# Kernel tuning notes

Measured on AMD Instinct MI355X. Metric: run time of the kernel, lower is better.

## Reference

```python
import jax, jax.numpy as jnp
import numpy as np

B = 8192
D_IN = 2048
MM = 1600
CHUNKS = 20
CS = MM // CHUNKS  # 80
D_OUT = 3000
EPS = 1e-12  # F.normalize clamp eps


def setup_inputs() -> dict:
    key = jax.random.key(0)
    ks = jax.random.split(key, 10)
    s_in = 1.0 / np.sqrt(D_IN)
    s_c = 1.0 / np.sqrt(CS)
    s_mm = 1.0 / np.sqrt(MM)
    return {
        "x0": jax.random.normal(ks[0], (B, D_IN), jnp.float32),
        "x1": jax.random.normal(ks[1], (B, D_IN), jnp.float32),
        "W0": jax.random.uniform(ks[2], (D_IN, MM), jnp.float32, -s_in, s_in),
        "b0": jax.random.uniform(ks[3], (MM,), jnp.float32, -s_in, s_in),
        "W1": jax.random.uniform(ks[4], (D_IN, MM), jnp.float32, -s_in, s_in),
        "b1": jax.random.uniform(ks[5], (MM,), jnp.float32, -s_in, s_in),
        # stacked bilinear weights: [chunks, out, in1, in2] like torch Bilinear
        "Wb": jax.random.uniform(ks[6], (CHUNKS, CS, CS, CS), jnp.float32, -s_c, s_c),
        "bb": jax.random.uniform(ks[7], (CHUNKS, CS), jnp.float32, -s_c, s_c),
        "Wout": jax.random.uniform(ks[8], (MM, D_OUT), jnp.float32, -s_mm, s_mm),
        "bout": jax.random.uniform(ks[9], (D_OUT,), jnp.float32, -s_mm, s_mm),
    }


def reference(x0, x1, W0, b0, W1, b1, Wb, bb, Wout, bout):
    # input projections: [B, MM]
    h0 = x0 @ W0 + b0
    h1 = x1 @ W1 + b1
    # split into equal chunks: [B, CHUNKS, CS]
    h0c = h0.reshape(B, CHUNKS, CS)
    h1c = h1.reshape(B, CHUNKS, CS)
    # batched bilinear over all chunks: z[b,c,o] = sum_{s,t} h0[b,c,s] Wb[c,o,s,t] h1[b,c,t] + bb[c,o]
    z = jnp.einsum('bcs,cost,bct->bco', h0c, Wb, h1c) + bb[None, :, :]
    # signed sqrt (pos_norm == 'before_cat')
    z = jnp.sqrt(jax.nn.relu(z)) - jnp.sqrt(jax.nn.relu(-z))
    # L2 normalize per chunk (torch F.normalize over dim=1 of the [B, CS] chunk)
    norm = jnp.linalg.norm(z, axis=-1, keepdims=True)
    z = z / jnp.maximum(norm, EPS)
    # concat chunks -> [B, MM], final projection
    z = z.reshape(B, MM)
    return z @ Wout + bout
```

## Files before the change

kernel.cpp:

```cpp
#include <hip/hip_runtime.h>
#include <hip/hip_bf16.h>

typedef unsigned short u16;
typedef unsigned int   u32;

using bf16x8 = __attribute__((ext_vector_type(8))) short;
using f32x4  = __attribute__((ext_vector_type(4))) float;
using fvec4  = __attribute__((ext_vector_type(4))) float;
using u16x4  = __attribute__((ext_vector_type(4))) unsigned short;

#define BSZ   8192
#define DIN   2048
#define MMD   1600
#define NCH   20
#define CSZ   80
#define DOUT  3000

__device__ __forceinline__ float bf2f(u16 u) {
    u32 x = ((u32)u) << 16; float f; __builtin_memcpy(&f, &x, 4); return f;
}
__device__ __forceinline__ u16 f2bf(float f) {
    u32 x; __builtin_memcpy(&x, &f, 4);
    u32 r = x + 0x7fffu + ((x >> 16) & 1u);
    return (u16)(r >> 16);
}

__device__ __forceinline__ void gl2lds16(const void* g, const void* l) {
    __builtin_amdgcn_global_load_lds(
        (const __attribute__((address_space(1))) u32*)g,
        (__attribute__((address_space(3))) u32*)l, 16, 0, 0);
}

__global__ void cast_bf16_k(const float* __restrict__ src, u16* __restrict__ dst, int n4) {
    int i = blockIdx.x * blockDim.x + threadIdx.x;
    if (i < n4) {
        fvec4 v = ((const fvec4*)src)[i];
        u16x4 o;
        o.x = f2bf(v.x); o.y = f2bf(v.y); o.z = f2bf(v.z); o.w = f2bf(v.w);
        ((u16x4*)dst)[i] = o;
    }
}

__global__ void transpose_cast_k(const float* __restrict__ src, u16* __restrict__ dst,
                                 int K, int N) {
    __shared__ float t[32][33];
    int k0 = blockIdx.x * 32, n0 = blockIdx.y * 32;
    int tx = threadIdx.x & 31, ty = threadIdx.x >> 5;
#pragma unroll
    for (int r = 0; r < 4; r++) {
        int n = n0 + tx;
        float v = (n < N) ? src[(size_t)(k0 + ty + 8 * r) * N + n] : 0.f;
        t[ty + 8 * r][tx] = v;
    }
    __syncthreads();
#pragma unroll
    for (int r = 0; r < 4; r++)
        dst[(size_t)(n0 + ty + 8 * r) * K + k0 + tx] = f2bf(t[tx][ty + 8 * r]);
}

template<bool OUT_BF16>
__global__ __launch_bounds__(256, 2) void gemm_bt_k(
    const u16* __restrict__ A, const u16* __restrict__ BT,
    const float* __restrict__ bias, void* __restrict__ C, int K, int N) {
    __shared__ __align__(16) u16 As[128 * 64];
    __shared__ __align__(16) u16 Bs[128 * 64];
    const int tid = threadIdx.x, w = tid >> 6, lane = tid & 63;
    const int lr = lane & 15, lk = lane >> 4, s7 = lr & 7;
    const int m0 = blockIdx.x * 128, n0 = blockIdx.y * 128;
    const int mh = (w >> 1) * 64, nh = (w & 1) * 64;
    const int so = (lane & 7) ^ (lane >> 3);
    int arow[4], brow[4];
#pragma unroll
    for (int i = 0; i < 4; i++) { arow[i] = (mh + i * 16 + lr) * 64; brow[i] = (nh + i * 16 + lr) * 64; }
    f32x4 acc[4][4] = {};
    const u16* Ag = A + (size_t)m0 * K;
    const u16* Bg = BT + (size_t)n0 * K;
    const int nslab = K >> 6;
    for (int kt = 0; kt < nslab; ++kt) {
        const int k0 = kt * 64;
        __syncthreads();
#pragma unroll
        for (int q = 0; q < 4; q++) {
            int ch = w * 4 + q;
            int row = ch * 8 + (lane >> 3);
            gl2lds16(Ag + (size_t)row * K + k0 + so * 8, As + ch * 512);
            gl2lds16(Bg + (size_t)row * K + k0 + so * 8, Bs + ch * 512);
        }
        __syncthreads();
#pragma unroll
        for (int ks = 0; ks < 64; ks += 32) {
            const int px = (((ks >> 3) + lk) ^ s7) * 8;
            bf16x8 av[4], bv[4];
#pragma unroll
            for (int i = 0; i < 4; i++) av[i] = *(const bf16x8*)(As + arow[i] + px);
#pragma unroll
            for (int j = 0; j < 4; j++) bv[j] = *(const bf16x8*)(Bs + brow[j] + px);
#pragma unroll
            for (int i = 0; i < 4; i++)
#pragma unroll
                for (int j = 0; j < 4; j++)
                    acc[i][j] = __builtin_amdgcn_mfma_f32_16x16x32_bf16(av[i], bv[j], acc[i][j], 0, 0, 0);
        }
    }
#pragma unroll
    for (int j = 0; j < 4; j++) {
        int n = n0 + nh + j * 16 + lr;
        if (n < N) {
            float bv = bias[n];
#pragma unroll
            for (int i = 0; i < 4; i++) {
                int mb = m0 + mh + i * 16 + lk * 4;
#pragma unroll
                for (int r = 0; r < 4; r++) {
                    float v = acc[i][j][r] + bv;
                    if (OUT_BF16) ((u16*)C)[(size_t)(mb + r) * N + n] = f2bf(v);
                    else          ((float*)C)[(size_t)(mb + r) * N + n] = v;
                }
            }
        }
    }
}

__global__ __launch_bounds__(256, 3) void bilinear_k(
    const u16* __restrict__ h0g, const u16* __restrict__ h1g,
    const u16* __restrict__ Wbg, const float* __restrict__ bbg,
    u16* __restrict__ zg) {
    __shared__ __align__(16) u16 h1s[128 * 96];
    __shared__ __align__(16) u16 Ws[CSZ * 96];
    const int tid = threadIdx.x, w = tid >> 6, lane = tid & 63;
    const int lr = lane & 15, lk = lane >> 4;
    const int m0 = blockIdx.x * 128, c = blockIdx.y;

    const u16* g1 = h1g + (size_t)m0 * MMD + c * CSZ;
#pragma unroll
    for (int it = 0; it < 6; ++it) {
        int oct = it * 256 + tid;
        int row = oct / 12, o = oct - row * 12;
        if (o < 10)
            gl2lds16(g1 + (size_t)row * MMD + o * 8, h1s + (it * 256 + w * 64) * 8);
    }
    {
        int oct = (tid >> 1) * 12 + 10 + (tid & 1);
        *(fvec4*)(h1s + oct * 8) = (fvec4){0.f, 0.f, 0.f, 0.f};
    }
    if (tid < 160) {
        int oct = (tid >> 1) * 12 + 10 + (tid & 1);
        *(fvec4*)(Ws + oct * 8) = (fvec4){0.f, 0.f, 0.f, 0.f};
    }

    const u16* WgBase = Wbg + (size_t)c * CSZ * 6400;
    const u16* wsrc[4];
    bool wok[4];
    int wdst[4];
#pragma unroll
    for (int it = 0; it < 4; ++it) {
        int oct = it * 256 + tid;
        int row = oct / 12, o = oct - row * 12;
        wok[it] = (oct < 960) && (o < 10);
        wsrc[it] = WgBase + (size_t)row * 6400 + o * 8;
        wdst[it] = (it * 256 + w * 64) * 8;
    }

    int aoff[2], boff[5];
#pragma unroll
    for (int i = 0; i < 2; ++i) aoff[i] = (w * 32 + i * 16 + lr) * 96 + lk * 8;
#pragma unroll
    for (int j = 0; j < 5; ++j) boff[j] = (j * 16 + lr) * 96 + lk * 8;

    const u16* hbase = h0g + (size_t)m0 * MMD + c * CSZ;
    int hoff[8];
#pragma unroll
    for (int i = 0; i < 2; ++i)
#pragma unroll
        for (int r = 0; r < 4; ++r)
            hoff[i * 4 + r] = (w * 32 + i * 16 + lk * 4 + r) * MMD;

    f32x4 z[2][5] = {};
    const f32x4 zf = {0.f, 0.f, 0.f, 0.f};

    for (int s = 0; s < 80; ++s) {
        __syncthreads();
#pragma unroll
        for (int it = 0; it < 4; ++it) {
            if (wok[it]) gl2lds16(wsrc[it], Ws + wdst[it]);
            wsrc[it] += CSZ;
        }
        u16 h0r[8];
        const u16* hs = hbase + s;
#pragma unroll
        for (int k = 0; k < 8; ++k) h0r[k] = hs[hoff[k]];
        __syncthreads();
        f32x4 P[2][5];
#pragma unroll
        for (int st = 0; st < 3; ++st) {
            bf16x8 av[2], bv[5];
#pragma unroll
            for (int i = 0; i < 2; ++i) av[i] = *(const bf16x8*)(h1s + aoff[i] + st * 32);
#pragma unroll
            for (int j = 0; j < 5; ++j) bv[j] = *(const bf16x8*)(Ws + boff[j] + st * 32);
#pragma unroll
            for (int i = 0; i < 2; ++i)
#pragma unroll
                for (int j = 0; j < 5; ++j)
                    P[i][j] = __builtin_amdgcn_mfma_f32_16x16x32_bf16(
                        av[i], bv[j], st == 0 ? zf : P[i][j], 0, 0, 0);
        }
#pragma unroll
        for (int i = 0; i < 2; ++i)
#pragma unroll
            for (int r = 0; r < 4; ++r) {
                float h0f = bf2f(h0r[i * 4 + r]);
#pragma unroll
                for (int j = 0; j < 5; ++j)
                    z[i][j][r] += h0f * P[i][j][r];
            }
    }

    float bbv[5];
#pragma unroll
    for (int j = 0; j < 5; j++) bbv[j] = bbg[c * CSZ + j * 16 + lr];
    float sq[2][4] = {};
#pragma unroll
    for (int i = 0; i < 2; i++)
#pragma unroll
        for (int j = 0; j < 5; j++)
#pragma unroll
            for (int r = 0; r < 4; r++) {
                float v = z[i][j][r] + bbv[j];
                float a = sqrtf(fabsf(v));
                v = (v < 0.f) ? -a : a;
                z[i][j][r] = v;
                sq[i][r] += v * v;
            }
#pragma unroll
    for (int d = 1; d < 16; d <<= 1)
#pragma unroll
        for (int i = 0; i < 2; i++)
#pragma unroll
            for (int r = 0; r < 4; r++)
                sq[i][r] += __shfl_xor(sq[i][r], d, 64);
    float sc[2][4];
#pragma unroll
    for (int i = 0; i < 2; i++)
#pragma unroll
        for (int r = 0; r < 4; r++)
            sc[i][r] = 1.f / fmaxf(sqrtf(sq[i][r]), 1e-12f);
#pragma unroll
    for (int i = 0; i < 2; i++)
#pragma unroll
        for (int r = 0; r < 4; r++) {
            int row = m0 + w * 32 + i * 16 + lk * 4 + r;
#pragma unroll
            for (int j = 0; j < 5; j++) {
                int col = c * CSZ + j * 16 + lr;
                zg[(size_t)row * MMD + col] = f2bf(z[i][j][r] * sc[i][r]);
            }
        }
}

extern "C" void kernel_launch(void* const* d_in, const int* in_sizes, int n_in,
                              void* d_out, int out_size, void* d_ws, size_t ws_size,
                              hipStream_t stream) {
    (void)in_sizes; (void)n_in; (void)out_size; (void)ws_size;
    const float* x0 = (const float*)d_in[0];
    const float* x1 = (const float*)d_in[1];
    const float* W0 = (const float*)d_in[2];
    const float* b0 = (const float*)d_in[3];
    const float* W1 = (const float*)d_in[4];
    const float* b1 = (const float*)d_in[5];
    const float* Wb = (const float*)d_in[6];
    const float* bb = (const float*)d_in[7];
    const float* Wo = (const float*)d_in[8];
    const float* bo = (const float*)d_in[9];

    char* ws = (char*)d_ws;
    size_t off = 0;
    auto alloc = [&](size_t bytes) { void* p = ws + off; off += (bytes + 255) & ~(size_t)255; return p; };
    u16* x0b = (u16*)alloc((size_t)BSZ * DIN * 2);
    u16* x1b = (u16*)alloc((size_t)BSZ * DIN * 2);
    u16* W0T = (u16*)alloc((size_t)1664 * DIN * 2);
    u16* W1T = (u16*)alloc((size_t)1664 * DIN * 2);
    u16* WbB = (u16*)alloc((size_t)NCH * CSZ * 6400 * 2);
    u16* WoT = (u16*)alloc((size_t)3072 * MMD * 2);
    u16* h0  = (u16*)alloc((size_t)BSZ * MMD * 2);
    u16* h1  = (u16*)alloc((size_t)BSZ * MMD * 2);
    u16* z   = x0b;

    cast_bf16_k<<<dim3(16384), dim3(256), 0, stream>>>(x0, x0b, (BSZ * DIN) / 4);
    cast_bf16_k<<<dim3(16384), dim3(256), 0, stream>>>(x1, x1b, (BSZ * DIN) / 4);
    cast_bf16_k<<<dim3(10000), dim3(256), 0, stream>>>(Wb, WbB, (NCH * CSZ * 6400) / 4);
    transpose_cast_k<<<dim3(DIN / 32, 1664 / 32), dim3(256), 0, stream>>>(W0, W0T, DIN, MMD);
    transpose_cast_k<<<dim3(DIN / 32, 1664 / 32), dim3(256), 0, stream>>>(W1, W1T, DIN, MMD);
    transpose_cast_k<<<dim3(MMD / 32, 3072 / 32), dim3(256), 0, stream>>>(Wo, WoT, MMD, DOUT);
    gemm_bt_k<true><<<dim3(BSZ / 128, 13), dim3(256), 0, stream>>>(x0b, W0T, b0, h0, DIN, MMD);
    gemm_bt_k<true><<<dim3(BSZ / 128, 13), dim3(256), 0, stream>>>(x1b, W1T, b1, h1, DIN, MMD);
    bilinear_k<<<dim3(BSZ / 128, NCH), dim3(256), 0, stream>>>(h0, h1, WbB, bb, z);
    gemm_bt_k<false><<<dim3(BSZ / 128, 24), dim3(256), 0, stream>>>(z, WoT, bo, d_out, MMD, DOUT);
}
```

Measured before the change: 755.0 us.

## Triple-buffer bilinear weight slices and keep h1 fragments in registers

The bilinear kernel now holds the h1 A-operand fragments in registers for the whole loop instead of staging them in LDS. It triple-buffers the per-step Wb slice in LDS with a padded row stride, prefetching the next slice and next h0 values while computing the current step. The two barriers per step become one barrier guarded by a manual vmcnt wait. The aim is to hide global-load latency and cut LDS traffic and bank conflicts, at the cost of more registers and a lower launch-bounds occupancy hint (3 to 2).

```diff
diff --git a/kernel.cpp b/kernel.cpp
--- a/kernel.cpp
+++ b/kernel.cpp
@@ -121,52 +121,40 @@
     }
 }
 
-__global__ __launch_bounds__(256, 3) void bilinear_k(
+__global__ __launch_bounds__(256, 2) void bilinear_k(
     const u16* __restrict__ h0g, const u16* __restrict__ h1g,
     const u16* __restrict__ Wbg, const float* __restrict__ bbg,
     u16* __restrict__ zg) {
-    __shared__ __align__(16) u16 h1s[128 * 96];
-    __shared__ __align__(16) u16 Ws[CSZ * 96];
+    constexpr int WROW = 104;
+    constexpr int WBUF = CSZ * WROW;
+    __shared__ __align__(16) u16 Ws[3 * WBUF];
     const int tid = threadIdx.x, w = tid >> 6, lane = tid & 63;
     const int lr = lane & 15, lk = lane >> 4;
     const int m0 = blockIdx.x * 128, c = blockIdx.y;
 
-    const u16* g1 = h1g + (size_t)m0 * MMD + c * CSZ;
-#pragma unroll
-    for (int it = 0; it < 6; ++it) {
-        int oct = it * 256 + tid;
-        int row = oct / 12, o = oct - row * 12;
-        if (o < 10)
-            gl2lds16(g1 + (size_t)row * MMD + o * 8, h1s + (it * 256 + w * 64) * 8);
-    }
-    {
-        int oct = (tid >> 1) * 12 + 10 + (tid & 1);
-        *(fvec4*)(h1s + oct * 8) = (fvec4){0.f, 0.f, 0.f, 0.f};
-    }
-    if (tid < 160) {
-        int oct = (tid >> 1) * 12 + 10 + (tid & 1);
-        *(fvec4*)(Ws + oct * 8) = (fvec4){0.f, 0.f, 0.f, 0.f};
+#pragma unroll
+    for (int t = 0; t < 2; ++t) {
+        int q = t * 256 + tid;
+        if (q < 480) {
+            int b = q / 160, r2 = q - b * 160;
+            *(fvec4*)(Ws + b * WBUF + (r2 >> 1) * WROW + 80 + (r2 & 1) * 8) =
+                (fvec4){0.f, 0.f, 0.f, 0.f};
+        }
     }
 
     const u16* WgBase = Wbg + (size_t)c * CSZ * 6400;
-    const u16* wsrc[4];
-    bool wok[4];
-    int wdst[4];
-#pragma unroll
-    for (int it = 0; it < 4; ++it) {
-        int oct = it * 256 + tid;
-        int row = oct / 12, o = oct - row * 12;
-        wok[it] = (oct < 960) && (o < 10);
+    const u16* wsrc[5];
+    bool wok[5];
+    int wdst[5];
+#pragma unroll
+    for (int it = 0; it < 5; ++it) {
+        int p = it * 256 + tid;
+        int row = p / 13, o = p - row * 13;
+        wok[it] = (p < 1040) && (o < 10);
         wsrc[it] = WgBase + (size_t)row * 6400 + o * 8;
         wdst[it] = (it * 256 + w * 64) * 8;
     }
 
-    int aoff[2], boff[5];
-#pragma unroll
-    for (int i = 0; i < 2; ++i) aoff[i] = (w * 32 + i * 16 + lr) * 96 + lk * 8;
-#pragma unroll
-    for (int j = 0; j < 5; ++j) boff[j] = (j * 16 + lr) * 96 + lk * 8;
-
     const u16* hbase = h0g + (size_t)m0 * MMD + c * CSZ;
     int hoff[8];
 #pragma unroll
@@ -175,35 +163,72 @@
         for (int r = 0; r < 4; ++r)
             hoff[i * 4 + r] = (w * 32 + i * 16 + lk * 4 + r) * MMD;
 
+#pragma unroll
+    for (int it = 0; it < 5; ++it) {
+        if (wok[it]) gl2lds16(wsrc[it], Ws + wdst[it]);
+        wsrc[it] += CSZ;
+    }
+    u16 h0r[8];
+#pragma unroll
+    for (int k = 0; k < 8; ++k) h0r[k] = hbase[hoff[k]];
+    const u16* hs = hbase + 1;
+
+    bf16x8 av[2][3];
+    const u16* h1base = h1g + (size_t)m0 * MMD + c * CSZ;
+#pragma unroll
+    for (int i = 0; i < 2; ++i) {
+        const u16* rowp = h1base + (size_t)(w * 32 + i * 16 + lr) * MMD;
+#pragma unroll
+        for (int st = 0; st < 3; ++st) {
+            if (st == 2 && lk >= 2) {
+                av[i][st] = (bf16x8){0, 0, 0, 0, 0, 0, 0, 0};
+            } else {
+                av[i][st] = *(const bf16x8*)(rowp + st * 32 + lk * 8);
+            }
+        }
+    }
+
+    __syncthreads();
+
+    int boff[5];
+#pragma unroll
+    for (int j = 0; j < 5; ++j) boff[j] = (j * 16 + lr) * WROW + lk * 8;
+
     f32x4 z[2][5] = {};
     const f32x4 zf = {0.f, 0.f, 0.f, 0.f};
-
+    int bufR = 0, bufW = 1;
+#pragma unroll 1
     for (int s = 0; s < 80; ++s) {
-        __syncthreads();
-#pragma unroll
-        for (int it = 0; it < 4; ++it) {
-            if (wok[it]) gl2lds16(wsrc[it], Ws + wdst[it]);
-            wsrc[it] += CSZ;
-        }
-        u16 h0r[8];
-        const u16* hs = hbase + s;
-#pragma unroll
-        for (int k = 0; k < 8; ++k) h0r[k] = hs[hoff[k]];
-        __syncthreads();
+        u16 h0n[8];
+        if (s < 79) {
+#pragma unroll
+            for (int it = 0; it < 5; ++it) {
+                if (wok[it]) gl2lds16(wsrc[it], Ws + bufW * WBUF + wdst[it]);
+                wsrc[it] += CSZ;
+            }
+#pragma unroll
+            for (int k = 0; k < 8; ++k) h0n[k] = hs[hoff[k]];
+            hs += 1;
+            asm volatile("s_waitcnt vmcnt(12)" ::: "memory");
+        } else {
+            asm volatile("s_waitcnt vmcnt(0)" ::: "memory");
+        }
+        __builtin_amdgcn_s_barrier();
+        asm volatile("" ::: "memory");
+
+        const u16* Wr = Ws + bufR * WBUF;
         f32x4 P[2][5];
 #pragma unroll
         for (int st = 0; st < 3; ++st) {
-            bf16x8 av[2], bv[5];
-#pragma unroll
-            for (int i = 0; i < 2; ++i) av[i] = *(const bf16x8*)(h1s + aoff[i] + st * 32);
-#pragma unroll
-            for (int j = 0; j < 5; ++j) bv[j] = *(const bf16x8*)(Ws + boff[j] + st * 32);
+            bf16x8 bv[5];
+#pragma unroll
+            for (int j = 0; j < 5; ++j) bv[j] = *(const bf16x8*)(Wr + boff[j] + st * 32);
 #pragma unroll
             for (int i = 0; i < 2; ++i)
 #pragma unroll
                 for (int j = 0; j < 5; ++j)
                     P[i][j] = __builtin_amdgcn_mfma_f32_16x16x32_bf16(
-                        av[i], bv[j], st == 0 ? zf : P[i][j], 0, 0, 0);
+                        av[i][st], bv[j], st == 0 ? zf : P[i][j], 0, 0, 0);
         }
 #pragma unroll
         for (int i = 0; i < 2; ++i)
@@ -214,6 +239,12 @@
                 for (int j = 0; j < 5; ++j)
                     z[i][j][r] += h0f * P[i][j][r];
             }
+        if (s < 79) {
+#pragma unroll
+            for (int k = 0; k < 8; ++k) h0r[k] = h0n[k];
+        }
+        bufR = (bufR == 2) ? 0 : bufR + 1;
+        bufW = (bufW == 2) ? 0 : bufW + 1;
     }
 
     float bbv[5];
```

Measured after the change: 731.1 us. 3.2% less time.
